# Kernel optimization log

Measured on AMD Instinct MI355X. Metric: run time of the kernel, lower is better.

## Reference

```python
import jax, jax.numpy as jnp
import numpy as np

N_NODES = 50000
N_EDGES = 800000
N_GRAPHS = 256
D_FEAT = 96
HIDDEN = 32


def setup_inputs() -> dict:
    key = jax.random.key(0)
    ks = jax.random.split(key, 8)
    x = jax.random.normal(ks[0], (N_NODES, D_FEAT), dtype=jnp.float32)
    edge_index = jax.random.randint(ks[1], (2, N_EDGES), 0, N_NODES, dtype=jnp.int64)
    batch = jnp.sort(jax.random.randint(ks[2], (N_NODES,), 0, N_GRAPHS, dtype=jnp.int64))
    W1 = jax.random.normal(ks[3], (D_FEAT, HIDDEN), dtype=jnp.float32) * 0.05
    b1 = jnp.zeros((HIDDEN,), dtype=jnp.float32)
    W2 = jax.random.normal(ks[4], (HIDDEN, HIDDEN), dtype=jnp.float32) * 0.05
    b2 = jnp.zeros((HIDDEN,), dtype=jnp.float32)
    Wc = jax.random.normal(ks[5], (HIDDEN, 2), dtype=jnp.float32) * 0.05
    bc = jnp.zeros((2,), dtype=jnp.float32)
    return {"x": x, "edge_index": edge_index, "batch": batch,
            "W1": W1, "b1": b1, "W2": W2, "b2": b2, "Wc": Wc, "bc": bc}


def reference(x, edge_index, batch, W1, b1, W2, b2, Wc, bc):
    src, dst = edge_index[0], edge_index[1]
    # GIN aggregation (eps=0): h_i = x_i + sum_{j -> i} x_j, scatter-add over edges
    agg = jax.ops.segment_sum(x[src], dst, num_segments=N_NODES)
    h = agg + x
    # 2-layer MLP inside GINConv
    h = jnp.maximum(h @ W1 + b1, 0.0) @ W2 + b2
    # outer ReLU (F.relu in forward)
    h = jnp.maximum(h, 0.0)
    # global mean pool per graph
    sums = jax.ops.segment_sum(h, batch, num_segments=N_GRAPHS)          # [G, H]
    counts = jax.ops.segment_sum(jnp.ones((N_NODES,), h.dtype), batch,
                                 num_segments=N_GRAPHS)                   # [G]
    pooled = sums / jnp.maximum(counts, 1.0)[:, None]
    return pooled @ Wc + bc  # [G, 2]
```

## Files before the change

### kernel.cpp

```cpp
#include <hip/hip_runtime.h>
#include <hip/hip_fp16.h>

#define N_NODES 50000
#define N_EDGES 800000
#define N_GRAPHS 256
#define D_FEAT 96
#define HIDDEN 32

#define NB 196
#define PB 400
#define PCHUNK 2000
#define SEGCAP 64
#define GWIN 16
#define LCAP 6400
#define XT 64
#define XBLK 782
#define XS_STRIDE 97
#define DUMMY_NODE N_NODES

__global__ void __launch_bounds__(256)
k_front(const float* __restrict__ x, const float* __restrict__ W1,
        __half* __restrict__ y16,
        const int* __restrict__ src, const int* __restrict__ dst,
        unsigned int* __restrict__ binned, unsigned short* __restrict__ cnt,
        float* __restrict__ sums, float* __restrict__ counts) {
    __shared__ __align__(16) char smem[26656];
    int blk = blockIdx.x;
    int tid = threadIdx.x;
    if (blk < PB) {
        unsigned int* q  = (unsigned int*)smem;
        int* qpos        = (int*)(smem + 25088);
        int* qflushed    = (int*)(smem + 25088 + 784);
        for (int i = tid; i < NB; i += 256) { qpos[i] = 0; qflushed[i] = 0; }
        __syncthreads();

        int e0 = blk * PCHUNK;
        for (int it = 0; it < PCHUNK; it += 256) {
            int idx = it + tid;
            if (idx < PCHUNK) {
                int e  = e0 + idx;
                int sn = src[e];
                int d  = dst[e];
                int b  = d >> 8;
                unsigned w = (unsigned)sn | ((unsigned)(d & 255) << 16);
                int pos = atomicAdd(&qpos[b], 1);
                q[b * 32 + (pos & 31)] = w;
            }
            __syncthreads();
            if (tid < NB) {
                int p  = qpos[tid];
                int fl = qflushed[tid];
                if (fl + 16 <= p && fl + 16 <= SEGCAP) {
                    unsigned int* qp = q + tid * 32;
                    do {
                        int base = fl & 31;
                        uint4 c0 = *(const uint4*)&qp[base];
                        uint4 c1 = *(const uint4*)&qp[base + 4];
                        uint4 c2 = *(const uint4*)&qp[base + 8];
                        uint4 c3 = *(const uint4*)&qp[base + 12];
                        uint4* gb = (uint4*)(binned +
                            ((size_t)tid * PB + blk) * SEGCAP + fl);
                        gb[0] = c0; gb[1] = c1; gb[2] = c2; gb[3] = c3;
                        fl += 16;
                    } while (fl + 16 <= p && fl + 16 <= SEGCAP);
                    qflushed[tid] = fl;
                }
            }
            __syncthreads();
        }
        if (tid < NB) {
            int p  = qpos[tid];
            int fl = qflushed[tid];
            int pcap = p < SEGCAP ? p : SEGCAP;
            cnt[tid * PB + blk] = (unsigned short)pcap;
            unsigned int* qp = q + tid * 32;
            while (fl < pcap) {
                int base = fl & 31;
                uint4 c0 = *(const uint4*)&qp[base];
                uint4 c1 = *(const uint4*)&qp[base + 4];
                uint4 c2 = *(const uint4*)&qp[base + 8];
                uint4 c3 = *(const uint4*)&qp[base + 12];
                uint4* gb = (uint4*)(binned +
                    ((size_t)tid * PB + blk) * SEGCAP + fl);
                gb[0] = c0; gb[1] = c1; gb[2] = c2; gb[3] = c3;
                fl += 16;
            }
        }
    } else {
        float* xs = (float*)smem;
        int xb = blk - PB;
        int n0 = xb * XT;
        int nn = N_NODES - n0; if (nn > XT) nn = XT;

        int gid = xb * 256 + tid;
        if (gid < N_GRAPHS * HIDDEN) sums[gid] = 0.f;
        if (gid < N_GRAPHS) counts[gid] = 0.f;
        if (xb == 0 && tid < HIDDEN)
            y16[(size_t)DUMMY_NODE * HIDDEN + tid] = __float2half(0.f);

        const float4* xsrc = (const float4*)(x + (size_t)n0 * D_FEAT);
        int nf4 = nn * (D_FEAT / 4);
        for (int idx = tid; idx < nf4; idx += 256) {
            int ln = (idx * 2731) >> 16;
            int k4 = idx - ln * 24;
            float4 v = xsrc[idx];
            float* dp = &xs[ln * XS_STRIDE + k4 * 4];
            dp[0] = v.x; dp[1] = v.y; dp[2] = v.z; dp[3] = v.w;
        }
        __syncthreads();

        int lane = tid & 63;
        int f0 = (tid >> 6) << 3;
        f0 = __builtin_amdgcn_readfirstlane(f0);

        if (lane < nn) {
            const float* xr = &xs[lane * XS_STRIDE];
            const float4* W1v = (const float4*)W1;
            float acc[8];
#pragma unroll
            for (int j = 0; j < 8; ++j) acc[j] = 0.f;
#pragma unroll
            for (int k = 0; k < D_FEAT; ++k) {
                float xv = xr[k];
                float4 wa = W1v[k * 8 + (f0 >> 2)];
                float4 wb = W1v[k * 8 + (f0 >> 2) + 1];
                acc[0] = fmaf(xv, wa.x, acc[0]);
                acc[1] = fmaf(xv, wa.y, acc[1]);
                acc[2] = fmaf(xv, wa.z, acc[2]);
                acc[3] = fmaf(xv, wa.w, acc[3]);
                acc[4] = fmaf(xv, wb.x, acc[4]);
                acc[5] = fmaf(xv, wb.y, acc[5]);
                acc[6] = fmaf(xv, wb.z, acc[6]);
                acc[7] = fmaf(xv, wb.w, acc[7]);
            }
            __half2 h01 = __floats2half2_rn(acc[0], acc[1]);
            __half2 h23 = __floats2half2_rn(acc[2], acc[3]);
            __half2 h45 = __floats2half2_rn(acc[4], acc[5]);
            __half2 h67 = __floats2half2_rn(acc[6], acc[7]);
            float4 pack;
            pack.x = __uint_as_float(*(const unsigned*)&h01);
            pack.y = __uint_as_float(*(const unsigned*)&h23);
            pack.z = __uint_as_float(*(const unsigned*)&h45);
            pack.w = __uint_as_float(*(const unsigned*)&h67);
            *(float4*)&y16[(size_t)(n0 + lane) * HIDDEN + f0] = pack;
        }
    }
}

__global__ void __launch_bounds__(1024)
k_agg(const unsigned int* __restrict__ binned, const unsigned short* __restrict__ cnt,
      const __half* __restrict__ y16, const int* __restrict__ batch,
      const float* __restrict__ b1, const float* __restrict__ W2,
      const float* __restrict__ b2,
      float* __restrict__ sums, float* __restrict__ counts) {
    __shared__ unsigned int list[LCAP];
    __shared__ unsigned short list2[LCAP];
    __shared__ unsigned int sA[512], sB[512];
    __shared__ unsigned short cs[PB];
    __shared__ unsigned int sOfs[PB];
    __shared__ unsigned int ncnt[256];
    __shared__ unsigned int offs[257];
    __shared__ unsigned int cur[256];
    __shared__ float w2s[HIDDEN * HIDDEN];
    __shared__ float accs[GWIN * HIDDEN];
    __shared__ float cntsl[GWIN];

    int tid = threadIdx.x;
    int bin = blockIdx.x;
    if (tid < 256) ncnt[tid] = 0;
    for (int i = tid; i < HIDDEN * HIDDEN; i += 1024) w2s[i] = W2[i];
    if (tid < GWIN * HIDDEN) accs[tid] = 0.f;
    if (tid < GWIN) cntsl[tid] = 0.f;
    if (tid < 512) {
        unsigned c = (tid < PB) ? (unsigned)cnt[bin * PB + tid] : 0u;
        if (tid < PB) cs[tid] = (unsigned short)c;
        sA[tid] = c;
    }
    __syncthreads();

    unsigned *ps = sA, *pd = sB;
    for (int d = 1; d < 512; d <<= 1) {
        if (tid < 512) { unsigned v = ps[tid]; if (tid >= d) v += ps[tid - d]; pd[tid] = v; }
        __syncthreads();
        unsigned* t = ps; ps = pd; pd = t;
    }
    if (tid < PB) sOfs[tid] = tid ? ps[tid - 1] : 0u;
    int ecount = (int)ps[PB - 1];
    if (ecount > LCAP) ecount = LCAP;
    __syncthreads();

    const unsigned int* ebase = binned + (size_t)bin * PB * SEGCAP;
    for (int idx = tid; idx < PB * SEGCAP; idx += 1024) {
        int s = idx >> 6;
        int i = idx & 63;
        if (i < (int)cs[s]) {
            unsigned pos = sOfs[s] + i;
            if (pos < LCAP) list[pos] = ebase[idx];
        }
    }
    __syncthreads();

    for (int e = tid; e < ecount; e += 1024)
        atomicAdd(&ncnt[list[e] >> 16], 1u);
    __syncthreads();

    if (tid < 256) sA[tid] = (ncnt[tid] + 7u) & ~7u;
    __syncthreads();
    ps = sA; pd = sB;
    for (int d = 1; d < 256; d <<= 1) {
        if (tid < 256) { unsigned v = ps[tid]; if (tid >= d) v += ps[tid - d]; pd[tid] = v; }
        __syncthreads();
        unsigned* t = ps; ps = pd; pd = t;
    }
    if (tid < 256) {
        offs[tid + 1] = ps[tid];
        cur[tid] = tid ? ps[tid - 1] : 0u;
    }
    if (tid == 0) offs[0] = 0;
    __syncthreads();

    for (int e = tid; e < ecount; e += 1024) {
        unsigned p = list[e];
        unsigned pos = atomicAdd(&cur[p >> 16], 1u);
        if (pos < LCAP) list2[pos] = (unsigned short)(p & 0xFFFFu);
    }
    __syncthreads();
    if (tid < 256) {
        unsigned i0 = cur[tid], i1 = offs[tid + 1];
        for (unsigned i = i0; i < i1 && i < LCAP; ++i)
            list2[i] = (unsigned short)DUMMY_NODE;
    }
    __syncthreads();

    int node0 = bin << 8;
    int nn = N_NODES - node0; if (nn > 256) nn = 256;
    int g = tid >> 5;
    int f = tid & 31;
    int gfirst = batch[node0];

    for (int ln = g * 8; ln < g * 8 + 8; ++ln) {
        if (ln >= nn) break;
        int node = node0 + ln;
        float acc = __half2float(y16[(size_t)node * HIDDEN + f]);
        int j = offs[ln], jend = offs[ln + 1];
        for (; j < jend; j += 8) {
            ushort4 qa = *(const ushort4*)&list2[j];
            ushort4 qb = *(const ushort4*)&list2[j + 4];
            float a0 = __half2float(y16[(size_t)qa.x * HIDDEN + f]);
            float a1 = __half2float(y16[(size_t)qa.y * HIDDEN + f]);
            float a2 = __half2float(y16[(size_t)qa.z * HIDDEN + f]);
            float a3 = __half2float(y16[(size_t)qa.w * HIDDEN + f]);
            float a4 = __half2float(y16[(size_t)qb.x * HIDDEN + f]);
            float a5 = __half2float(y16[(size_t)qb.y * HIDDEN + f]);
            float a6 = __half2float(y16[(size_t)qb.z * HIDDEN + f]);
            float a7 = __half2float(y16[(size_t)qb.w * HIDDEN + f]);
            acc += ((a0 + a1) + (a2 + a3)) + ((a4 + a5) + (a6 + a7));
        }

        float h1 = fmaxf(acc + b1[f], 0.f);
        float h2 = b2[f];
#pragma unroll
        for (int k = 0; k < HIDDEN; ++k)
            h2 = fmaf(__shfl(h1, k, 32), w2s[k * HIDDEN + f], h2);
        float h = fmaxf(h2, 0.f);

        int gr = batch[node];
        int b = gr - gfirst;
        if (b < GWIN) {
            atomicAdd(&accs[b * HIDDEN + f], h);
            if (f == 0) atomicAdd(&cntsl[b], 1.f);
        } else {
            atomicAdd(&sums[(size_t)gr * HIDDEN + f], h);
            if (f == 0) atomicAdd(&counts[gr], 1.f);
        }
    }
    __syncthreads();

    for (int i = tid; i < GWIN * HIDDEN; i += 1024) {
        float v = accs[i];
        if (v != 0.f) atomicAdd(&sums[(size_t)gfirst * HIDDEN + i], v);
    }
    if (tid < GWIN) {
        float c = cntsl[tid];
        if (c != 0.f) atomicAdd(&counts[gfirst + tid], c);
    }
}

__global__ void k_out(const float* __restrict__ sums, const float* __restrict__ counts,
                      const float* __restrict__ Wc, const float* __restrict__ bc,
                      float* __restrict__ out) {
    int g = threadIdx.x;
    if (g >= N_GRAPHS) return;
    float inv = 1.f / fmaxf(counts[g], 1.f);
    float o0 = bc[0], o1 = bc[1];
#pragma unroll
    for (int k = 0; k < HIDDEN; ++k) {
        float p = sums[(size_t)g * HIDDEN + k] * inv;
        o0 = fmaf(p, Wc[k * 2 + 0], o0);
        o1 = fmaf(p, Wc[k * 2 + 1], o1);
    }
    out[g * 2 + 0] = o0;
    out[g * 2 + 1] = o1;
}

extern "C" void kernel_launch(void* const* d_in, const int* in_sizes, int n_in,
                              void* d_out, int out_size, void* d_ws, size_t ws_size,
                              hipStream_t stream) {
    const float* x     = (const float*)d_in[0];
    const int*   ei    = (const int*)d_in[1];
    const int*   batch = (const int*)d_in[2];
    const float* W1    = (const float*)d_in[3];
    const float* b1    = (const float*)d_in[4];
    const float* W2    = (const float*)d_in[5];
    const float* b2    = (const float*)d_in[6];
    const float* Wc    = (const float*)d_in[7];
    const float* bc    = (const float*)d_in[8];
    float* out = (float*)d_out;

    char* ws = (char*)d_ws;
    float*          sums   = (float*)ws;
    float*          counts = (float*)(ws + 32768);
    unsigned short* cnt    = (unsigned short*)(ws + 33792);
    unsigned int*   binned = (unsigned int*)(ws + 190592);
    __half*         y16    = (__half*)(ws + 20260992);

    k_front<<<PB + XBLK, 256, 0, stream>>>(
        x, W1, y16, ei, ei + N_EDGES, binned, cnt, sums, counts);

    k_agg<<<NB, 1024, 0, stream>>>(binned, cnt, y16, batch,
                                   b1, W2, b2, sums, counts);

    k_out<<<1, 256, 0, stream>>>(sums, counts, Wc, bc, out);
}
```

Measured before the change: 133.5 us.

## Split each aggregation bin across two blocks and drop intermediate edge list

k_agg now launches two blocks per 256-node bin, each handling 128 destination nodes, so twice as many workgroups run on the GPU. The staging list, its 400-entry prefix scan and the copy into shared memory are removed. Instead each block reads the binned global segment twice, once to count per-node degrees and once to scatter source indices into the CSR list. This roughly halves per-block shared memory and gives more parallelism for the gather phase. The cost is that every block reads the whole bin's edge data from global twice, and each bin's edges are read by two blocks. Biases are also staged in shared memory.

```diff
diff --git a/kernel.cpp b/kernel.cpp
--- a/kernel.cpp
+++ b/kernel.cpp
@@ -12,7 +12,8 @@
 #define PCHUNK 2000
 #define SEGCAP 64
 #define GWIN 16
-#define LCAP 6400
+#define HN 128
+#define HCAP 3200
 #define XT 64
 #define XBLK 782
 #define XS_STRIDE 97
@@ -153,96 +154,89 @@
       const float* __restrict__ b1, const float* __restrict__ W2,
       const float* __restrict__ b2,
       float* __restrict__ sums, float* __restrict__ counts) {
-    __shared__ unsigned int list[LCAP];
-    __shared__ unsigned short list2[LCAP];
-    __shared__ unsigned int sA[512], sB[512];
+    __shared__ unsigned short list2[HCAP];
     __shared__ unsigned short cs[PB];
-    __shared__ unsigned int sOfs[PB];
-    __shared__ unsigned int ncnt[256];
-    __shared__ unsigned int offs[257];
-    __shared__ unsigned int cur[256];
+    __shared__ unsigned int ncnt[HN];
+    __shared__ unsigned int sA[HN], sB[HN];
+    __shared__ unsigned int offs[HN + 1];
+    __shared__ unsigned int cur[HN];
     __shared__ float w2s[HIDDEN * HIDDEN];
+    __shared__ float b1s[HIDDEN], b2s[HIDDEN];
     __shared__ float accs[GWIN * HIDDEN];
     __shared__ float cntsl[GWIN];
 
-    int tid = threadIdx.x;
-    int bin = blockIdx.x;
-    if (tid < 256) ncnt[tid] = 0;
-    for (int i = tid; i < HIDDEN * HIDDEN; i += 1024) w2s[i] = W2[i];
+    int tid  = threadIdx.x;
+    int bin  = blockIdx.x >> 1;
+    int nlo  = (blockIdx.x & 1) << 7;
+
+    if (tid < HN) ncnt[tid] = 0;
+    w2s[tid & 1023] = W2[tid & 1023];
+    if (tid < HIDDEN) { b1s[tid] = b1[tid]; b2s[tid] = b2[tid]; }
     if (tid < GWIN * HIDDEN) accs[tid] = 0.f;
     if (tid < GWIN) cntsl[tid] = 0.f;
-    if (tid < 512) {
-        unsigned c = (tid < PB) ? (unsigned)cnt[bin * PB + tid] : 0u;
-        if (tid < PB) cs[tid] = (unsigned short)c;
-        sA[tid] = c;
-    }
-    __syncthreads();
-
-    unsigned *ps = sA, *pd = sB;
-    for (int d = 1; d < 512; d <<= 1) {
-        if (tid < 512) { unsigned v = ps[tid]; if (tid >= d) v += ps[tid - d]; pd[tid] = v; }
-        __syncthreads();
-        unsigned* t = ps; ps = pd; pd = t;
-    }
-    if (tid < PB) sOfs[tid] = tid ? ps[tid - 1] : 0u;
-    int ecount = (int)ps[PB - 1];
-    if (ecount > LCAP) ecount = LCAP;
+    if (tid < PB) cs[tid] = cnt[bin * PB + tid];
     __syncthreads();
 
     const unsigned int* ebase = binned + (size_t)bin * PB * SEGCAP;
+
     for (int idx = tid; idx < PB * SEGCAP; idx += 1024) {
         int s = idx >> 6;
         int i = idx & 63;
         if (i < (int)cs[s]) {
-            unsigned pos = sOfs[s] + i;
-            if (pos < LCAP) list[pos] = ebase[idx];
-        }
-    }
-    __syncthreads();
-
-    for (int e = tid; e < ecount; e += 1024)
-        atomicAdd(&ncnt[list[e] >> 16], 1u);
-    __syncthreads();
-
-    if (tid < 256) sA[tid] = (ncnt[tid] + 7u) & ~7u;
-    __syncthreads();
-    ps = sA; pd = sB;
-    for (int d = 1; d < 256; d <<= 1) {
-        if (tid < 256) { unsigned v = ps[tid]; if (tid >= d) v += ps[tid - d]; pd[tid] = v; }
+            unsigned p = ebase[idx];
+            int d = (int)(p >> 16) - nlo;
+            if ((unsigned)d < HN) atomicAdd(&ncnt[d], 1u);
+        }
+    }
+    __syncthreads();
+
+    if (tid < HN) sA[tid] = (ncnt[tid] + 7u) & ~7u;
+    __syncthreads();
+    unsigned *ps = sA, *pd = sB;
+    for (int d = 1; d < HN; d <<= 1) {
+        if (tid < HN) { unsigned v = ps[tid]; if (tid >= d) v += ps[tid - d]; pd[tid] = v; }
         __syncthreads();
         unsigned* t = ps; ps = pd; pd = t;
     }
-    if (tid < 256) {
+    if (tid < HN) {
         offs[tid + 1] = ps[tid];
         cur[tid] = tid ? ps[tid - 1] : 0u;
     }
     if (tid == 0) offs[0] = 0;
     __syncthreads();
 
-    for (int e = tid; e < ecount; e += 1024) {
-        unsigned p = list[e];
-        unsigned pos = atomicAdd(&cur[p >> 16], 1u);
-        if (pos < LCAP) list2[pos] = (unsigned short)(p & 0xFFFFu);
-    }
-    __syncthreads();
-    if (tid < 256) {
+    for (int idx = tid; idx < PB * SEGCAP; idx += 1024) {
+        int s = idx >> 6;
+        int i = idx & 63;
+        if (i < (int)cs[s]) {
+            unsigned p = ebase[idx];
+            int d = (int)(p >> 16) - nlo;
+            if ((unsigned)d < HN) {
+                unsigned pos = atomicAdd(&cur[d], 1u);
+                if (pos < HCAP) list2[pos] = (unsigned short)(p & 0xFFFFu);
+            }
+        }
+    }
+    __syncthreads();
+    if (tid < HN) {
         unsigned i0 = cur[tid], i1 = offs[tid + 1];
-        for (unsigned i = i0; i < i1 && i < LCAP; ++i)
+        for (unsigned i = i0; i < i1 && i < HCAP; ++i)
             list2[i] = (unsigned short)DUMMY_NODE;
     }
     __syncthreads();
 
-    int node0 = bin << 8;
-    int nn = N_NODES - node0; if (nn > 256) nn = 256;
+    int node0 = (bin << 8) + nlo;
+    int nn = N_NODES - node0; if (nn > HN) nn = HN;
     int g = tid >> 5;
     int f = tid & 31;
-    int gfirst = batch[node0];
-
-    for (int ln = g * 8; ln < g * 8 + 8; ++ln) {
+    int gfirst = (node0 < N_NODES) ? batch[node0] : 0;
+
+    for (int ln = g * 4; ln < g * 4 + 4; ++ln) {
         if (ln >= nn) break;
         int node = node0 + ln;
         float acc = __half2float(y16[(size_t)node * HIDDEN + f]);
-        int j = offs[ln], jend = offs[ln + 1];
+        int j = offs[ln];
+        int jend = offs[ln + 1]; if (jend > HCAP) jend = HCAP;
         for (; j < jend; j += 8) {
             ushort4 qa = *(const ushort4*)&list2[j];
             ushort4 qb = *(const ushort4*)&list2[j + 4];
@@ -257,8 +251,8 @@
             acc += ((a0 + a1) + (a2 + a3)) + ((a4 + a5) + (a6 + a7));
         }
 
-        float h1 = fmaxf(acc + b1[f], 0.f);
-        float h2 = b2[f];
+        float h1 = fmaxf(acc + b1s[f], 0.f);
+        float h2 = b2s[f];
 #pragma unroll
         for (int k = 0; k < HIDDEN; ++k)
             h2 = fmaf(__shfl(h1, k, 32), w2s[k * HIDDEN + f], h2);
@@ -327,8 +321,8 @@
     k_front<<<PB + XBLK, 256, 0, stream>>>(
         x, W1, y16, ei, ei + N_EDGES, binned, cnt, sums, counts);
 
-    k_agg<<<NB, 1024, 0, stream>>>(binned, cnt, y16, batch,
-                                   b1, W2, b2, sums, counts);
+    k_agg<<<NB * 2, 1024, 0, stream>>>(binned, cnt, y16, batch,
+                                       b1, W2, b2, sums, counts);
 
     k_out<<<1, 256, 0, stream>>>(sums, counts, Wc, bc, out);
 }
```

After: 154.3 us. 1.16x slower.
